# Performance work log

Measured on AMD Instinct MI355X. Metric: run time of the kernel, lower is better.

The kernel has to match this reference:

```python
import jax, jax.numpy as jnp
import numpy as np

POOL_LIST = (1, 2, 4)  # pyramid levels -> 1x1, 2x2, 4x4 bins


def _spp_mix(x, pool_list=POOL_LIST):
    """Spatial pyramid pooling, pool_type='mix' (max + mean), channels_last.

    x: (B, H, W, C) -> (B, sum(p*p for p in pool_list) * C)
    Matches the original TF loop ordering: for each level, outer loop over
    bin columns (jy), inner loop over bin rows (ix).
    """
    B, H, W, C = x.shape
    outs = []
    for p in pool_list:
        wr, wc = H // p, W // p  # window rows/cols (floor div, as in original)
        # crop to covered region, then split into p x p bins in one reshape
        xs = x[:, :p * wr, :p * wc, :].reshape(B, p, wr, p, wc, C)
        # mix = max + mean over each window
        v = xs.max(axis=(2, 4)) + xs.mean(axis=(2, 4))  # (B, pr, pc, C)
        # original appends in (jy outer, ix inner) order -> transpose rows/cols
        v = jnp.transpose(v, (0, 2, 1, 3)).reshape(B, p * p * C)
        outs.append(v)
    return jnp.concatenate(outs, axis=-1)


def setup_inputs() -> dict:
    key = jax.random.key(0)
    x = jax.random.normal(key, (32, 64, 64, 512), dtype=jnp.float32)
    return {"x": x}


def reference(x) -> jnp.ndarray:
    return _spp_mix(x)
```

## Files before the change

### kernel.cpp

```cpp
#include <hip/hip_runtime.h>
#include <math.h>


#define B_ 32
#define HW_ 64
#define C_ 512
#define CVEC 128

__device__ __forceinline__ float4 f4max(float4 a, float4 b) {
    return make_float4(fmaxf(a.x, b.x), fmaxf(a.y, b.y),
                       fmaxf(a.z, b.z), fmaxf(a.w, b.w));
}
__device__ __forceinline__ float4 f4add(float4 a, float4 b) {
    return make_float4(a.x + b.x, a.y + b.y, a.z + b.z, a.w + b.w);
}
__device__ __forceinline__ float4 f4mix(float4 m, float4 s, float inv) {
    return make_float4(m.x + s.x * inv, m.y + s.y * inv,
                       m.z + s.z * inv, m.w + s.w * inv);
}

__global__ __launch_bounds__(512) void spp_fused_kernel(
    const float4* __restrict__ x,
    float4* __restrict__ maxbuf,
    float4* __restrict__ sumbuf,
    unsigned int* counters,
    float4* __restrict__ out)
{
    const int blk = blockIdx.x;
    const int b   = blk >> 4;
    const int bin = blk & 15;
    const int br  = bin >> 2;
    const int bc  = bin & 3;
    const int tid = threadIdx.x;
    const int cg  = tid & (CVEC - 1);
    const int q   = tid >> 7;

    const int base = ((b * HW_ + br * 16 + q * 4) * HW_ + bc * 16) * CVEC + cg;

    float4 mx = make_float4(-INFINITY, -INFINITY, -INFINITY, -INFINITY);
    float4 sm = make_float4(0.f, 0.f, 0.f, 0.f);

    #pragma unroll 8
    for (int k = 0; k < 64; ++k) {
        const int r = k >> 4;
        const int j = k & 15;
        const float4 v = x[base + (r * HW_ + j) * CVEC];
        mx = f4max(mx, v);
        sm = f4add(sm, v);
    }

    __shared__ float4 smax[3][CVEC];
    __shared__ float4 ssum[3][CVEC];
    __shared__ int lastflag;

    if (q > 0) { smax[q - 1][cg] = mx; ssum[q - 1][cg] = sm; }
    __syncthreads();
    if (q == 0) {
        mx = f4max(f4max(mx, smax[0][cg]), f4max(smax[1][cg], smax[2][cg]));
        sm = f4add(f4add(sm, ssum[0][cg]), f4add(ssum[1][cg], ssum[2][cg]));
        const int o = (b * 16 + bin) * CVEC + cg;
        maxbuf[o] = mx;
        sumbuf[o] = sm;
        out[b * (21 * CVEC) + 5 * CVEC + (bc * 4 + br) * CVEC + cg] =
            f4mix(mx, sm, 1.0f / 256.0f);
        __threadfence();
    }
    __syncthreads();

    if (tid == 0) {
        unsigned int ret = atomicInc(&counters[b * 64], 15u);
        lastflag = (ret == 14u) ? 1 : 0;
    }
    __syncthreads();

    if (lastflag && tid < CVEC) {
        __threadfence();
        const int pbase = b * 16 * CVEC + cg;
        const int row   = b * (21 * CVEC);
        float4 m1 = make_float4(-INFINITY, -INFINITY, -INFINITY, -INFINITY);
        float4 s1 = make_float4(0.f, 0.f, 0.f, 0.f);
        #pragma unroll
        for (int pr = 0; pr < 2; ++pr) {
            #pragma unroll
            for (int pc = 0; pc < 2; ++pc) {
                float4 mm = make_float4(-INFINITY, -INFINITY, -INFINITY, -INFINITY);
                float4 ss = make_float4(0.f, 0.f, 0.f, 0.f);
                #pragma unroll
                for (int dr = 0; dr < 2; ++dr) {
                    #pragma unroll
                    for (int dc = 0; dc < 2; ++dc) {
                        const int bb = (2 * pr + dr) * 4 + (2 * pc + dc);
                        mm = f4max(mm, maxbuf[pbase + bb * CVEC]);
                        ss = f4add(ss, sumbuf[pbase + bb * CVEC]);
                    }
                }
                out[row + CVEC + (pc * 2 + pr) * CVEC + cg] =
                    f4mix(mm, ss, 1.0f / 1024.0f);
                m1 = f4max(m1, mm);
                s1 = f4add(s1, ss);
            }
        }
        out[row + cg] = f4mix(m1, s1, 1.0f / 4096.0f);
    }
}

extern "C" void kernel_launch(void* const* d_in, const int* in_sizes, int n_in,
                              void* d_out, int out_size, void* d_ws, size_t ws_size,
                              hipStream_t stream) {
    const float4* x = (const float4*)d_in[0];
    float* ws = (float*)d_ws;
    float4* maxbuf = (float4*)ws;
    float4* sumbuf = (float4*)(ws + B_ * 16 * C_);
    unsigned int* counters = (unsigned int*)(ws + 2 * B_ * 16 * C_);
    float4* out = (float4*)d_out;

    spp_fused_kernel<<<B_ * 16, 512, 0, stream>>>(x, maxbuf, sumbuf, counters, out);
}
```

Measured before the change: 414.6 us.

## Split SPP into row-reduce, bin-reduce and aggregate kernels

The single fused kernel, which used atomic last-block detection, is replaced by three kernels. The first reads each image row contiguously across 2048 blocks and writes per-row, per-column-bin partials. The second reduces 16 rows into each 4x4 bin, and the third builds the 2x2 and 1x1 levels. The aim is more parallelism and contiguous reads during the dominant 256 MB input pass, and removal of the atomics and fences. The cost is extra intermediate traffic (about 16 MB written and read back) plus two more kernel launches.

```diff
diff --git a/kernel.cpp b/kernel.cpp
--- a/kernel.cpp
+++ b/kernel.cpp
@@ -19,11 +19,52 @@
                        m.z + s.z * inv, m.w + s.w * inv);
 }
 
-__global__ __launch_bounds__(512) void spp_fused_kernel(
+__global__ __launch_bounds__(256) void spp_rows_kernel(
     const float4* __restrict__ x,
-    float4* __restrict__ maxbuf,
-    float4* __restrict__ sumbuf,
-    unsigned int* counters,
+    float4* __restrict__ rmax,
+    float4* __restrict__ rsum)
+{
+    const int blk = blockIdx.x;
+    const int t   = threadIdx.x;
+    const float4* row = x + (size_t)blk * (HW_ * CVEC);
+
+    float4 m[4], s[4];
+    #pragma unroll
+    for (int bc = 0; bc < 4; ++bc) {
+        m[bc] = make_float4(-INFINITY, -INFINITY, -INFINITY, -INFINITY);
+        s[bc] = make_float4(0.f, 0.f, 0.f, 0.f);
+        #pragma unroll
+        for (int k8 = 0; k8 < 8; ++k8) {
+            const float4 v = row[(bc * 8 + k8) * 256 + t];
+            m[bc] = f4max(m[bc], v);
+            s[bc] = f4add(s[bc], v);
+        }
+    }
+
+    __shared__ float4 lm[4][CVEC];
+    __shared__ float4 ls[4][CVEC];
+    if (t >= CVEC) {
+        #pragma unroll
+        for (int bc = 0; bc < 4; ++bc) { lm[bc][t - CVEC] = m[bc]; ls[bc][t - CVEC] = s[bc]; }
+    }
+    __syncthreads();
+    if (t < CVEC) {
+        #pragma unroll
+        for (int bc = 0; bc < 4; ++bc) {
+            m[bc] = f4max(m[bc], lm[bc][t]);
+            s[bc] = f4add(s[bc], ls[bc][t]);
+            const int o = (blk * 4 + bc) * CVEC + t;
+            rmax[o] = m[bc];
+            rsum[o] = s[bc];
+        }
+    }
+}
+
+__global__ __launch_bounds__(256) void spp_bins_kernel(
+    const float4* __restrict__ rmax,
+    const float4* __restrict__ rsum,
+    float4* __restrict__ bmax,
+    float4* __restrict__ bsum,
     float4* __restrict__ out)
 {
     const int blk = blockIdx.x;
@@ -31,77 +72,70 @@
     const int bin = blk & 15;
     const int br  = bin >> 2;
     const int bc  = bin & 3;
-    const int tid = threadIdx.x;
-    const int cg  = tid & (CVEC - 1);
-    const int q   = tid >> 7;
+    const int t   = threadIdx.x;
+    const int cg  = t & (CVEC - 1);
+    const int ih  = t >> 7;
 
-    const int base = ((b * HW_ + br * 16 + q * 4) * HW_ + bc * 16) * CVEC + cg;
-
-    float4 mx = make_float4(-INFINITY, -INFINITY, -INFINITY, -INFINITY);
-    float4 sm = make_float4(0.f, 0.f, 0.f, 0.f);
-
-    #pragma unroll 8
-    for (int k = 0; k < 64; ++k) {
-        const int r = k >> 4;
-        const int j = k & 15;
-        const float4 v = x[base + (r * HW_ + j) * CVEC];
-        mx = f4max(mx, v);
-        sm = f4add(sm, v);
+    float4 m = make_float4(-INFINITY, -INFINITY, -INFINITY, -INFINITY);
+    float4 s = make_float4(0.f, 0.f, 0.f, 0.f);
+    #pragma unroll
+    for (int r = 0; r < 8; ++r) {
+        const int i = br * 16 + ih * 8 + r;
+        const int o = ((b * HW_ + i) * 4 + bc) * CVEC + cg;
+        m = f4max(m, rmax[o]);
+        s = f4add(s, rsum[o]);
     }
 
-    __shared__ float4 smax[3][CVEC];
-    __shared__ float4 ssum[3][CVEC];
-    __shared__ int lastflag;
+    __shared__ float4 lm[CVEC];
+    __shared__ float4 ls[CVEC];
+    if (ih) { lm[cg] = m; ls[cg] = s; }
+    __syncthreads();
+    if (!ih) {
+        m = f4max(m, lm[cg]);
+        s = f4add(s, ls[cg]);
+        const int o = (b * 16 + bin) * CVEC + cg;
+        bmax[o] = m;
+        bsum[o] = s;
+        out[b * (21 * CVEC) + 5 * CVEC + (bc * 4 + br) * CVEC + cg] =
+            f4mix(m, s, 1.0f / 256.0f);
+    }
+}
 
-    if (q > 0) { smax[q - 1][cg] = mx; ssum[q - 1][cg] = sm; }
-    __syncthreads();
-    if (q == 0) {
-        mx = f4max(f4max(mx, smax[0][cg]), f4max(smax[1][cg], smax[2][cg]));
-        sm = f4add(f4add(sm, ssum[0][cg]), f4add(ssum[1][cg], ssum[2][cg]));
-        const int o = (b * 16 + bin) * CVEC + cg;
-        maxbuf[o] = mx;
-        sumbuf[o] = sm;
-        out[b * (21 * CVEC) + 5 * CVEC + (bc * 4 + br) * CVEC + cg] =
-            f4mix(mx, sm, 1.0f / 256.0f);
-        __threadfence();
+__global__ __launch_bounds__(256) void spp_agg_kernel(
+    const float4* __restrict__ bmax,
+    const float4* __restrict__ bsum,
+    float4* __restrict__ out)
+{
+    const int idx = blockIdx.x * 256 + threadIdx.x;
+    const int b   = idx >> 7;
+    const int cg  = idx & (CVEC - 1);
+    const int pbase = b * 16 * CVEC + cg;
+    const int row   = b * (21 * CVEC);
+
+    float4 m1 = make_float4(-INFINITY, -INFINITY, -INFINITY, -INFINITY);
+    float4 s1 = make_float4(0.f, 0.f, 0.f, 0.f);
+    #pragma unroll
+    for (int pr = 0; pr < 2; ++pr) {
+        #pragma unroll
+        for (int pc = 0; pc < 2; ++pc) {
+            float4 mm = make_float4(-INFINITY, -INFINITY, -INFINITY, -INFINITY);
+            float4 ss = make_float4(0.f, 0.f, 0.f, 0.f);
+            #pragma unroll
+            for (int dr = 0; dr < 2; ++dr) {
+                #pragma unroll
+                for (int dc = 0; dc < 2; ++dc) {
+                    const int bb = (2 * pr + dr) * 4 + (2 * pc + dc);
+                    mm = f4max(mm, bmax[pbase + bb * CVEC]);
+                    ss = f4add(ss, bsum[pbase + bb * CVEC]);
+                }
+            }
+            out[row + CVEC + (pc * 2 + pr) * CVEC + cg] =
+                f4mix(mm, ss, 1.0f / 1024.0f);
+            m1 = f4max(m1, mm);
+            s1 = f4add(s1, ss);
+        }
     }
-    __syncthreads();
-
-    if (tid == 0) {
-        unsigned int ret = atomicInc(&counters[b * 64], 15u);
-        lastflag = (ret == 14u) ? 1 : 0;
-    }
-    __syncthreads();
-
-    if (lastflag && tid < CVEC) {
-        __threadfence();
-        const int pbase = b * 16 * CVEC + cg;
-        const int row   = b * (21 * CVEC);
-        float4 m1 = make_float4(-INFINITY, -INFINITY, -INFINITY, -INFINITY);
-        float4 s1 = make_float4(0.f, 0.f, 0.f, 0.f);
-        #pragma unroll
-        for (int pr = 0; pr < 2; ++pr) {
-            #pragma unroll
-            for (int pc = 0; pc < 2; ++pc) {
-                float4 mm = make_float4(-INFINITY, -INFINITY, -INFINITY, -INFINITY);
-                float4 ss = make_float4(0.f, 0.f, 0.f, 0.f);
-                #pragma unroll
-                for (int dr = 0; dr < 2; ++dr) {
-                    #pragma unroll
-                    for (int dc = 0; dc < 2; ++dc) {
-                        const int bb = (2 * pr + dr) * 4 + (2 * pc + dc);
-                        mm = f4max(mm, maxbuf[pbase + bb * CVEC]);
-                        ss = f4add(ss, sumbuf[pbase + bb * CVEC]);
-                    }
-                }
-                out[row + CVEC + (pc * 2 + pr) * CVEC + cg] =
-                    f4mix(mm, ss, 1.0f / 1024.0f);
-                m1 = f4max(m1, mm);
-                s1 = f4add(s1, ss);
-            }
-        }
-        out[row + cg] = f4mix(m1, s1, 1.0f / 4096.0f);
-    }
+    out[row + cg] = f4mix(m1, s1, 1.0f / 4096.0f);
 }
 
 extern "C" void kernel_launch(void* const* d_in, const int* in_sizes, int n_in,
@@ -109,10 +143,13 @@
                               hipStream_t stream) {
     const float4* x = (const float4*)d_in[0];
     float* ws = (float*)d_ws;
-    float4* maxbuf = (float4*)ws;
-    float4* sumbuf = (float4*)(ws + B_ * 16 * C_);
-    unsigned int* counters = (unsigned int*)(ws + 2 * B_ * 16 * C_);
+    float4* rmax = (float4*)ws;
+    float4* rsum = (float4*)(ws + (size_t)B_ * HW_ * 4 * C_);
+    float4* bmax = (float4*)(ws + (size_t)2 * B_ * HW_ * 4 * C_);
+    float4* bsum = (float4*)(ws + (size_t)2 * B_ * HW_ * 4 * C_ + B_ * 16 * C_);
     float4* out = (float4*)d_out;
 
-    spp_fused_kernel<<<B_ * 16, 512, 0, stream>>>(x, maxbuf, sumbuf, counters, out);
+    spp_rows_kernel<<<B_ * HW_, 256, 0, stream>>>(x, rmax, rsum);
+    spp_bins_kernel<<<B_ * 16, 256, 0, stream>>>(rmax, rsum, bmax, bsum, out);
+    spp_agg_kernel<<<(B_ * CVEC) / 256, 256, 0, stream>>>(bmax, bsum, out);
 }
```

Result: faster. 369.5 us (-10.9%).
